# Kernel tuning notes

Hardware: AMD Instinct MI355X
Metric: run time of the kernel (lower is better)

## Reference

```python
import jax, jax.numpy as jnp
import numpy as np

B, N_LATENT, N_NUISANCE, N_OUT = 2048, 64, 16, 2048


def setup_inputs() -> dict:
    key = jax.random.key(0)
    ks = jax.random.split(key, 6)
    z = jax.random.normal(ks[0], (B, N_LATENT + N_NUISANCE), dtype=jnp.float32)
    size_factor = jax.random.uniform(ks[1], (B, 1), dtype=jnp.float32) + 0.5
    # nn.Linear(n_latent, n_out, bias=False): store as [L, O] for z0 @ W
    amat_w = jax.random.normal(ks[2], (N_LATENT, N_OUT), dtype=jnp.float32) / np.sqrt(N_LATENT).astype(np.float32)
    amat_site = jax.random.normal(ks[3], (N_NUISANCE, N_LATENT, N_OUT), dtype=jnp.float32)
    offsets = jax.random.normal(ks[4], (N_NUISANCE, N_OUT), dtype=jnp.float32)
    px_r = jax.random.normal(ks[5], (N_OUT,), dtype=jnp.float32)
    return {"z": z, "size_factor": size_factor, "amat_w": amat_w,
            "amat_site": amat_site, "offsets": offsets, "px_r": px_r}


def reference(z, size_factor, amat_w, amat_site, offsets, px_r):
    n_nuisance = offsets.shape[0]
    nuisance_oh = z[..., -n_nuisance:]          # [B, N] one-hot site indicator
    z0 = z[..., :-n_nuisance]                   # [B, L] latent part
    x1 = z0 @ amat_w                            # [B, O] shared linear decoder
    nuisance_ids = jnp.argmax(nuisance_oh, axis=-1)  # [B] int ids
    # dropout(p=0.1) in eval mode == identity; .detach() -> stop_gradient
    z0_d = jax.lax.stop_gradient(z0)
    As = amat_site[nuisance_ids]                # [B, L, O] per-sample gathered weights
    x2 = jnp.einsum('bl,blo->bo', z0_d, As)     # batched matvec reduction over L
    mu = jax.nn.softmax(x1 + x2 + offsets[nuisance_ids], axis=-1)  # [B, O]
    mu = mu * size_factor                       # scale by per-cell size factor
    theta = jnp.exp(px_r)                       # NB inverse-dispersion, [O]
    return mu, theta
```

## Files before the change

kernel.cpp:

```cpp
#include <hip/hip_runtime.h>
#include <hip/hip_bf16.h>

#define NB 2048
#define NL 64
#define NN 16
#define NROW 80
#define NO 2048
#define TPB 256
#define OPT 8
#define G 8
#define CHUNKS (NB / G)
#define MBLK (NN * NL * NO / 4 / TPB)

typedef unsigned int   u32;
typedef unsigned short u16;

__device__ __forceinline__ float bflo(u32 u) { union { u32 i; float f; } c; c.i = u << 16;          return c.f; }
__device__ __forceinline__ float bfhi(u32 u) { union { u32 i; float f; } c; c.i = u & 0xffff0000u;  return c.f; }
__device__ __forceinline__ u16 f2bf(float f) { __hip_bfloat16 h = __float2bfloat16(f); return *(u16*)&h; }

__global__ __launch_bounds__(TPB) void prep(
    const float* __restrict__ W,
    const float* __restrict__ A,
    const float* __restrict__ z,
    const float* __restrict__ pxr,
    u16* __restrict__ M,
    u32* __restrict__ counts,
    u32* __restrict__ perm,
    float* __restrict__ out)
{
    const int blk = blockIdx.x;
    const int tid = threadIdx.x;

    if (blk < MBLK) {
        size_t t    = (size_t)blk * TPB + tid;
        size_t base = t * 4;
        float4 w = *(const float4*)(W + (base & (size_t)(NL * NO - 1)));
        float4 a = *(const float4*)(A + base);
        ushort4 m;
        m.x = f2bf(w.x + a.x);
        m.y = f2bf(w.y + a.y);
        m.z = f2bf(w.z + a.z);
        m.w = f2bf(w.w + a.w);
        *(ushort4*)(M + base) = m;
        return;
    }

    if (blk == MBLK) {
        __shared__ u32 lc[NN];
        if (tid < NN) lc[tid] = 0;
        __syncthreads();
        #pragma unroll
        for (int k = 0; k < NB / TPB; ++k) {
            const int b = k * TPB + tid;
            const float* zp = z + (size_t)b * NROW + NL;
            float4 v0 = *(const float4*)(zp);
            float4 v1 = *(const float4*)(zp + 4);
            float4 v2 = *(const float4*)(zp + 8);
            float4 v3 = *(const float4*)(zp + 12);
            float best = v0.x; int bi = 0;
            #define CK(val, idx) if ((val) > best) { best = (val); bi = (idx); }
            CK(v0.y, 1)  CK(v0.z, 2)  CK(v0.w, 3)
            CK(v1.x, 4)  CK(v1.y, 5)  CK(v1.z, 6)  CK(v1.w, 7)
            CK(v2.x, 8)  CK(v2.y, 9)  CK(v2.z, 10) CK(v2.w, 11)
            CK(v3.x, 12) CK(v3.y, 13) CK(v3.z, 14) CK(v3.w, 15)
            #undef CK
            u32 pos = atomicAdd(&lc[bi], 1u);
            perm[(u32)bi * NB + pos] = (u32)b;
        }
        __syncthreads();
        if (tid < NN) counts[tid] = lc[tid];
        return;
    }

    for (int o = tid; o < NO; o += TPB)
        out[(size_t)NB * NO + o] = __expf(pxr[o]);
}

__global__ __launch_bounds__(TPB) void decoder_g(
    const float* __restrict__ z,
    const float* __restrict__ sf,
    const u16*   __restrict__ M,
    const float* __restrict__ offs,
    const u32*   __restrict__ counts,
    const u32*   __restrict__ perm,
    float* __restrict__ out)
{
    const int bucket = blockIdx.x / CHUNKS;
    const int chunk  = blockIdx.x % CHUNKS;
    const u32 cnt    = counts[bucket];
    if ((u32)(chunk * G) >= cnt) return;
    const int tid = threadIdx.x;

    __shared__ float zt[NL][G];
    __shared__ float s_sf[G];
    __shared__ u32   s_rows[G];
    __shared__ float s_red[2][G][4];

    if (tid < G) {
        u32 idx = (u32)(chunk * G + tid);
        u32 clamped = idx < cnt ? idx : (cnt - 1u);
        u32 r = perm[(size_t)bucket * NB + clamped];
        s_rows[tid] = r;
        s_sf[tid]   = sf[r];
    }
    __syncthreads();
    {
        const int l = tid & (NL - 1);
        const int g = tid >> 6;
        u32 r0 = s_rows[g], r1 = s_rows[g + 4];
        zt[l][g]     = z[(size_t)r0 * NROW + l];
        zt[l][g + 4] = z[(size_t)r1 * NROW + l];
    }
    __syncthreads();

    const int o0 = tid * OPT;
    const uint4* mv = (const uint4*)(M + (size_t)bucket * (NL * NO) + o0);

    float acc[G][OPT];
    {
        float4 oa = *(const float4*)(offs + bucket * NO + o0);
        float4 ob = *(const float4*)(offs + bucket * NO + o0 + 4);
        #pragma unroll
        for (int g = 0; g < G; ++g) {
            acc[g][0] = oa.x; acc[g][1] = oa.y; acc[g][2] = oa.z; acc[g][3] = oa.w;
            acc[g][4] = ob.x; acc[g][5] = ob.y; acc[g][6] = ob.z; acc[g][7] = ob.w;
        }
    }

    #pragma unroll 8
    for (int l = 0; l < NL; ++l) {
        const uint4 m = mv[l * (NO / OPT)];
        float v[OPT];
        v[0] = bflo(m.x); v[1] = bfhi(m.x);
        v[2] = bflo(m.y); v[3] = bfhi(m.y);
        v[4] = bflo(m.z); v[5] = bfhi(m.z);
        v[6] = bflo(m.w); v[7] = bfhi(m.w);
        const float4 za = *(const float4*)(&zt[l][0]);
        const float4 zb = *(const float4*)(&zt[l][4]);
        const float zg[G] = { za.x, za.y, za.z, za.w, zb.x, zb.y, zb.z, zb.w };
        #pragma unroll
        for (int g = 0; g < G; ++g)
            #pragma unroll
            for (int j = 0; j < OPT; ++j)
                acc[g][j] += zg[g] * v[j];
    }

    const int wv = tid >> 6;
    #pragma unroll
    for (int g = 0; g < G; ++g) {
        float m = acc[g][0];
        #pragma unroll
        for (int j = 1; j < OPT; ++j) m = fmaxf(m, acc[g][j]);
        #pragma unroll
        for (int off = 32; off > 0; off >>= 1) m = fmaxf(m, __shfl_down(m, off));
        if ((tid & 63) == 0) s_red[0][g][wv] = m;
    }
    __syncthreads();
    float mx[G];
    #pragma unroll
    for (int g = 0; g < G; ++g)
        mx[g] = fmaxf(fmaxf(s_red[0][g][0], s_red[0][g][1]),
                      fmaxf(s_red[0][g][2], s_red[0][g][3]));

    #pragma unroll
    for (int g = 0; g < G; ++g) {
        float s = 0.f;
        #pragma unroll
        for (int j = 0; j < OPT; ++j) { acc[g][j] = __expf(acc[g][j] - mx[g]); s += acc[g][j]; }
        #pragma unroll
        for (int off = 32; off > 0; off >>= 1) s += __shfl_down(s, off);
        if ((tid & 63) == 0) s_red[1][g][wv] = s;
    }
    __syncthreads();
    #pragma unroll
    for (int g = 0; g < G; ++g) {
        if ((u32)(chunk * G + g) < cnt) {
            const float sm  = (s_red[1][g][0] + s_red[1][g][1]) + (s_red[1][g][2] + s_red[1][g][3]);
            const float scl = s_sf[g] / sm;
            float* op = out + (size_t)s_rows[g] * NO + o0;
            *(float4*)(op)     = make_float4(acc[g][0] * scl, acc[g][1] * scl, acc[g][2] * scl, acc[g][3] * scl);
            *(float4*)(op + 4) = make_float4(acc[g][4] * scl, acc[g][5] * scl, acc[g][6] * scl, acc[g][7] * scl);
        }
    }
}

__global__ __launch_bounds__(TPB) void decoder_f(
    const float* __restrict__ z, const float* __restrict__ sf,
    const float* __restrict__ W, const float* __restrict__ A,
    const float* __restrict__ offs, const float* __restrict__ pxr,
    float* __restrict__ out)
{
    const int b   = blockIdx.x;
    const int tid = threadIdx.x;
    if (b == NB) {
        for (int o = tid; o < NO; o += TPB)
            out[(size_t)NB * NO + o] = __expf(pxr[o]);
        return;
    }
    __shared__ float z0s[NL];
    __shared__ int   s_id;
    __shared__ float s_red[6];
    if (tid < NL) z0s[tid] = z[b * NROW + tid];
    if (tid == 0) {
        float best = -1e30f; int bi = 0;
        for (int i = 0; i < NN; ++i) {
            float v = z[b * NROW + NL + i];
            if (v > best) { best = v; bi = i; }
        }
        s_id = bi;
    }
    __syncthreads();
    const int id = s_id;
    const int o0 = tid * OPT;
    const float* wp = W + o0;
    const float* ap = A + (size_t)id * NL * NO + o0;
    float acc[OPT];
    {
        float4 oa = *(const float4*)(offs + id * NO + o0);
        float4 ob = *(const float4*)(offs + id * NO + o0 + 4);
        acc[0] = oa.x; acc[1] = oa.y; acc[2] = oa.z; acc[3] = oa.w;
        acc[4] = ob.x; acc[5] = ob.y; acc[6] = ob.z; acc[7] = ob.w;
    }
    #pragma unroll 4
    for (int l = 0; l < NL; ++l) {
        const float zl = z0s[l];
        float4 w0 = *(const float4*)(wp + l * NO);
        float4 w1 = *(const float4*)(wp + l * NO + 4);
        float4 a0 = *(const float4*)(ap + l * NO);
        float4 a1 = *(const float4*)(ap + l * NO + 4);
        acc[0] += zl * (w0.x + a0.x); acc[1] += zl * (w0.y + a0.y);
        acc[2] += zl * (w0.z + a0.z); acc[3] += zl * (w0.w + a0.w);
        acc[4] += zl * (w1.x + a1.x); acc[5] += zl * (w1.y + a1.y);
        acc[6] += zl * (w1.z + a1.z); acc[7] += zl * (w1.w + a1.w);
    }
    float m = acc[0];
    #pragma unroll
    for (int j = 1; j < OPT; ++j) m = fmaxf(m, acc[j]);
    #pragma unroll
    for (int off = 32; off > 0; off >>= 1) m = fmaxf(m, __shfl_down(m, off));
    if ((tid & 63) == 0) s_red[tid >> 6] = m;
    __syncthreads();
    if (tid == 0) s_red[4] = fmaxf(fmaxf(s_red[0], s_red[1]), fmaxf(s_red[2], s_red[3]));
    __syncthreads();
    const float mx = s_red[4];
    float ex[OPT];
    float s = 0.f;
    #pragma unroll
    for (int j = 0; j < OPT; ++j) { ex[j] = __expf(acc[j] - mx); s += ex[j]; }
    #pragma unroll
    for (int off = 32; off > 0; off >>= 1) s += __shfl_down(s, off);
    if ((tid & 63) == 0) s_red[tid >> 6] = s;
    __syncthreads();
    if (tid == 0) s_red[5] = (s_red[0] + s_red[1]) + (s_red[2] + s_red[3]);
    __syncthreads();
    const float scale = sf[b] / s_red[5];
    float* op = out + (size_t)b * NO + o0;
    *(float4*)(op)     = make_float4(ex[0] * scale, ex[1] * scale, ex[2] * scale, ex[3] * scale);
    *(float4*)(op + 4) = make_float4(ex[4] * scale, ex[5] * scale, ex[6] * scale, ex[7] * scale);
}

extern "C" void kernel_launch(void* const* d_in, const int* in_sizes, int n_in,
                              void* d_out, int out_size, void* d_ws, size_t ws_size,
                              hipStream_t stream) {
    const float* z    = (const float*)d_in[0];
    const float* sf   = (const float*)d_in[1];
    const float* W    = (const float*)d_in[2];
    const float* A    = (const float*)d_in[3];
    const float* offs = (const float*)d_in[4];
    const float* pxr  = (const float*)d_in[5];
    float* out = (float*)d_out;

    const size_t m_bytes = (size_t)NN * NL * NO * sizeof(u16);
    const size_t need    = m_bytes + 256 + (size_t)NN * NB * sizeof(u32);
    if (ws_size >= need) {
        u16* M      = (u16*)d_ws;
        u32* counts = (u32*)((char*)d_ws + m_bytes);
        u32* perm   = (u32*)((char*)d_ws + m_bytes + 256);
        hipLaunchKernelGGL(prep, dim3(MBLK + 2), dim3(TPB), 0, stream,
                           W, A, z, pxr, M, counts, perm, out);
        hipLaunchKernelGGL(decoder_g, dim3(NN * CHUNKS), dim3(TPB), 0, stream,
                           z, sf, M, offs, counts, perm, out);
    } else {
        hipLaunchKernelGGL(decoder_f, dim3(NB + 1), dim3(TPB), 0, stream,
                           z, sf, W, A, offs, pxr, out);
    }
}
```

Measured before the change: 111.9 us.

## Launch decoder over compact bucket worklist and halve rows per block

The prep kernel now builds a compact worklist of (bucket, chunk) pairs and a total count. The decoder then launches only that many live blocks instead of a dense bucket-by-chunk grid where most blocks exit immediately. Rows per block drop from 8 to 4, which roughly doubles the number of active blocks to fill more CUs. The cost is twice as many reads of each bucket's weight slice from cache, and a serial prefix sum in one thread of prep.

```diff
diff --git a/kernel.cpp b/kernel.cpp
--- a/kernel.cpp
+++ b/kernel.cpp
@@ -8,8 +8,8 @@
 #define NO 2048
 #define TPB 256
 #define OPT 8
-#define G 8
-#define CHUNKS (NB / G)
+#define G 4
+#define MAXWL (NB / G + NN)
 #define MBLK (NN * NL * NO / 4 / TPB)
 
 typedef unsigned int   u32;
@@ -27,6 +27,8 @@
     u16* __restrict__ M,
     u32* __restrict__ counts,
     u32* __restrict__ perm,
+    u32* __restrict__ wl,
+    u32* __restrict__ nit,
     float* __restrict__ out)
 {
     const int blk = blockIdx.x;
@@ -48,6 +50,7 @@
 
     if (blk == MBLK) {
         __shared__ u32 lc[NN];
+        __shared__ u32 choff[NN + 1];
         if (tid < NN) lc[tid] = 0;
         __syncthreads();
         #pragma unroll
@@ -69,7 +72,19 @@
             perm[(u32)bi * NB + pos] = (u32)b;
         }
         __syncthreads();
-        if (tid < NN) counts[tid] = lc[tid];
+        if (tid == 0) {
+            u32 n = 0;
+            for (int i = 0; i < NN; ++i) { choff[i] = n; n += (lc[i] + G - 1) / G; }
+            choff[NN] = n;
+            nit[0] = n;
+        }
+        __syncthreads();
+        if (tid < NN) {
+            counts[tid] = lc[tid];
+            const u32 nch = (lc[tid] + G - 1) / G;
+            const u32 off = choff[tid];
+            for (u32 c = 0; c < nch; ++c) wl[off + c] = ((u32)tid << 16) | c;
+        }
         return;
     }
 
@@ -84,13 +99,16 @@
     const float* __restrict__ offs,
     const u32*   __restrict__ counts,
     const u32*   __restrict__ perm,
+    const u32*   __restrict__ wl,
+    const u32*   __restrict__ nit,
     float* __restrict__ out)
 {
-    const int bucket = blockIdx.x / CHUNKS;
-    const int chunk  = blockIdx.x % CHUNKS;
+    if (blockIdx.x >= nit[0]) return;
+    const u32 w      = wl[blockIdx.x];
+    const int bucket = (int)(w >> 16);
+    const int chunk  = (int)(w & 0xffffu);
     const u32 cnt    = counts[bucket];
-    if ((u32)(chunk * G) >= cnt) return;
-    const int tid = threadIdx.x;
+    const int tid    = threadIdx.x;
 
     __shared__ float zt[NL][G];
     __shared__ float s_sf[G];
@@ -108,9 +126,7 @@
     {
         const int l = tid & (NL - 1);
         const int g = tid >> 6;
-        u32 r0 = s_rows[g], r1 = s_rows[g + 4];
-        zt[l][g]     = z[(size_t)r0 * NROW + l];
-        zt[l][g + 4] = z[(size_t)r1 * NROW + l];
+        zt[l][g] = z[(size_t)s_rows[g] * NROW + l];
     }
     __syncthreads();
 
@@ -137,8 +153,7 @@
         v[4] = bflo(m.z); v[5] = bfhi(m.z);
         v[6] = bflo(m.w); v[7] = bfhi(m.w);
         const float4 za = *(const float4*)(&zt[l][0]);
-        const float4 zb = *(const float4*)(&zt[l][4]);
-        const float zg[G] = { za.x, za.y, za.z, za.w, zb.x, zb.y, zb.z, zb.w };
+        const float zg[G] = { za.x, za.y, za.z, za.w };
         #pragma unroll
         for (int g = 0; g < G; ++g)
             #pragma unroll
@@ -272,15 +287,18 @@
     float* out = (float*)d_out;
 
     const size_t m_bytes = (size_t)NN * NL * NO * sizeof(u16);
-    const size_t need    = m_bytes + 256 + (size_t)NN * NB * sizeof(u32);
+    const size_t p_bytes = (size_t)NN * NB * sizeof(u32);
+    const size_t need    = m_bytes + 256 + p_bytes + (MAXWL + 64) * sizeof(u32);
     if (ws_size >= need) {
         u16* M      = (u16*)d_ws;
         u32* counts = (u32*)((char*)d_ws + m_bytes);
         u32* perm   = (u32*)((char*)d_ws + m_bytes + 256);
+        u32* wl     = (u32*)((char*)d_ws + m_bytes + 256 + p_bytes);
+        u32* nit    = wl + MAXWL;
         hipLaunchKernelGGL(prep, dim3(MBLK + 2), dim3(TPB), 0, stream,
-                           W, A, z, pxr, M, counts, perm, out);
-        hipLaunchKernelGGL(decoder_g, dim3(NN * CHUNKS), dim3(TPB), 0, stream,
-                           z, sf, M, offs, counts, perm, out);
+                           W, A, z, pxr, M, counts, perm, wl, nit, out);
+        hipLaunchKernelGGL(decoder_g, dim3(MAXWL), dim3(TPB), 0, stream,
+                           z, sf, M, offs, counts, perm, wl, nit, out);
     } else {
         hipLaunchKernelGGL(decoder_f, dim3(NB + 1), dim3(TPB), 0, stream,
                            z, sf, W, A, offs, pxr, out);
```

New measurement: 107.6 us. 3.8% less time.
